# Kernel tuning notes

Hardware: AMD Instinct MI355X
Metric: run time of the kernel (lower is better)

The kernel has to match this reference:

```python
import jax, jax.numpy as jnp
import numpy as np

K = 8          # num groups
SIZE = 250     # state/hidden size (h1 = h2 = 250)
M = 576        # flattened input size (24x24)
B = 2048       # batch
HA = 100       # attention hidden
EPS = 1e-5


def _ln(x, g, b):
    mu = jnp.mean(x, axis=-1, keepdims=True)
    v = jnp.mean(jnp.square(x - mu), axis=-1, keepdims=True)
    return (x - mu) * jax.lax.rsqrt(v + EPS) * g + b


def setup_inputs() -> dict:
    key = jax.random.key(0)
    ks = jax.random.split(key, 10)
    def w(k, shape):
        return jax.random.normal(k, shape, jnp.float32) / np.sqrt(shape[0]).astype(np.float32)
    inp = {
        "x": jax.random.normal(ks[0], (B * K, M), jnp.float32),
        "state": jax.random.normal(ks[1], (B * K, SIZE), jnp.float32),
        # encoder: Linear(SIZE,250) + ReLU + LN(250)
        "enc_W": w(ks[2], (SIZE, 250)), "enc_b": jnp.zeros((250,), jnp.float32),
        "enc_g": jnp.ones((250,), jnp.float32), "enc_bt": jnp.zeros((250,), jnp.float32),
        # core: Linear(500,250) + ReLU + LN(250)
        "core_W": w(ks[3], (500, 250)), "core_b": jnp.zeros((250,), jnp.float32),
        "core_g": jnp.ones((250,), jnp.float32), "core_bt": jnp.zeros((250,), jnp.float32),
        # context: Linear(250,250) + ReLU + LN(250)
        "ctx_W": w(ks[4], (250, 250)), "ctx_b": jnp.zeros((250,), jnp.float32),
        "ctx_g": jnp.ones((250,), jnp.float32), "ctx_bt": jnp.zeros((250,), jnp.float32),
        # attention: Linear(250,100)+Tanh+LN(100)+Linear(100,1)+Sigmoid
        "att_W1": w(ks[5], (250, HA)), "att_b1": jnp.zeros((HA,), jnp.float32),
        "att_g": jnp.ones((HA,), jnp.float32), "att_bt": jnp.zeros((HA,), jnp.float32),
        "att_W2": w(ks[6], (HA, 1)), "att_b2": jnp.zeros((1,), jnp.float32),
        # output: Linear(250 + 250 + M, SIZE)
        "out_W": w(ks[7], (250 + 250 + M, SIZE)), "out_b": jnp.zeros((SIZE,), jnp.float32),
    }
    return inp


def reference(x, state, enc_W, enc_b, enc_g, enc_bt, core_W, core_b, core_g, core_bt,
              ctx_W, ctx_b, ctx_g, ctx_bt, att_W1, att_b1, att_g, att_bt,
              att_W2, att_b2, out_W, out_b):
    bk = state.shape[0]
    b = bk // K
    h1 = 250
    # 0-1. encode state -> [B*K, h1]
    s1 = _ln(jax.nn.relu(state @ enc_W + enc_b), enc_g, enc_bt)
    s1r = s1.reshape(b, K, h1)
    # 2-3. focus / context pairs via static gather index [K, K-1]
    idx = np.array([[j for j in range(K) if j != i] for i in range(K)], np.int32)
    cs = s1r[:, idx]                                    # [b, K, K-1, h1]
    fs = jnp.broadcast_to(s1r[:, :, None, :], cs.shape)  # [b, K, K-1, h1]
    # 4. concat pairs -> [b*K*(K-1), 2*h1]
    concat = jnp.concatenate([fs, cs], axis=-1).reshape(b * K * (K - 1), 2 * h1)
    # 5. core MLP
    core_out = _ln(jax.nn.relu(concat @ core_W + core_b), core_g, core_bt)
    # context MLP
    context_out = _ln(jax.nn.relu(core_out @ ctx_W + ctx_b), ctx_g, ctx_bt)
    # attention scalar per pair
    att_h = _ln(jnp.tanh(core_out @ att_W1 + att_b1), att_g, att_bt)
    att = jax.nn.sigmoid(att_h @ att_W2 + att_b2)        # [b*K*(K-1), 1]
    # 6-7. attention-weighted sum over K-1 context effects -> [B*K, h2]
    effect_sum = jnp.sum(context_out.reshape(bk, K - 1, h1) * att.reshape(bk, K - 1, 1), axis=1)
    # 8. decode
    total = jnp.concatenate([s1, effect_sum, x], axis=1)  # [B*K, h1+h2+M]
    new_state = total @ out_W + out_b                     # [B*K, SIZE]
    return new_state
```

## Files before the change

kernel.cpp:

```cpp
#include <hip/hip_runtime.h>
#include <math.h>

#define KK 8
#define H 250
#define MDIM 576
#define NB 2048
#define HA 100
#define ROWS (NB*KK)
#define PROWS (ROWS*7)
#define PQS 512
#define KP 1088
#define CSLD 352
#define EPS 1e-5f

typedef unsigned short ushort_t;
typedef short short8 __attribute__((ext_vector_type(8)));
typedef unsigned short us8 __attribute__((ext_vector_type(8)));
typedef unsigned short us4 __attribute__((ext_vector_type(4)));
typedef unsigned short us2 __attribute__((ext_vector_type(2)));
typedef float f32x4 __attribute__((ext_vector_type(4)));

__device__ __forceinline__ void wave_reduce2(float& a, float& b) {
#pragma unroll
    for (int m = 1; m < 64; m <<= 1) {
        a += __shfl_xor(a, m, 64);
        b += __shfl_xor(b, m, 64);
    }
}
__device__ __forceinline__ float wave_reduce1(float a) {
#pragma unroll
    for (int m = 1; m < 64; m <<= 1) a += __shfl_xor(a, m, 64);
    return a;
}

__device__ __forceinline__ void async_copy16(const void* g, void* l) {
    __builtin_amdgcn_global_load_lds(
        (const __attribute__((address_space(1))) void*)g,
        (__attribute__((address_space(3))) void*)l, 16, 0, 0);
}

__device__ __forceinline__ ushort_t f2bf(float v) {
    union { float f; unsigned int u; } c; c.f = v;
    unsigned int x = c.u;
    x += 0x7fff + ((x >> 16) & 1);
    return (ushort_t)(x >> 16);
}
__device__ __forceinline__ float bf2f(ushort_t v) {
    union { unsigned int u; float f; } c; c.u = ((unsigned int)v) << 16;
    return c.f;
}

__global__ __launch_bounds__(256) void k_prep(
    const float* __restrict__ out_W, const float* __restrict__ core_W,
    const float* __restrict__ ctx_W, const float* __restrict__ att_W1,
    const float* __restrict__ enc_W, const float* __restrict__ state,
    const float* __restrict__ x,
    ushort_t* __restrict__ Wt, ushort_t* __restrict__ Wpq,
    ushort_t* __restrict__ Wca, ushort_t* __restrict__ Wenc,
    ushort_t* __restrict__ Sb, ushort_t* __restrict__ Abuf)
{
    const int b = blockIdx.x, t = threadIdx.x;
    if (b < 256) {
        const int n = b;
        for (int k = t; k < KP; k += 256) {
            const float v = (n < H && k < 1076) ? out_W[(size_t)k * H + n] : 0.f;
            Wt[(size_t)n * KP + k] = f2bf(v);
        }
    } else if (b < 768) {
        const int n = b - 256, k = t;
        float v = 0.f;
        if (k < H) {
            if (n < H)                    v = core_W[(size_t)k * H + n];
            else if (n >= 256 && n < 506) v = core_W[(size_t)(H + k) * H + (n - 256)];
        }
        Wpq[(size_t)n * 256 + k] = f2bf(v);
    } else if (b < 1152) {
        const int n = b - 768, k = t;
        float v = 0.f;
        if (k < H) {
            if (n < H)           v = ctx_W[(size_t)k * H + n];
            else if (n < H + HA) v = att_W1[(size_t)k * HA + (n - H)];
        }
        Wca[(size_t)n * 256 + k] = f2bf(v);
    } else if (b < 1408) {
        const int n = b - 1152, k = t;
        const float v = (n < H && k < H) ? enc_W[(size_t)k * H + n] : 0.f;
        Wenc[(size_t)n * 256 + k] = f2bf(v);
    } else if (b < 2432) {
        const int r0 = (b - 1408) * 16;
        for (int idx = t; idx < 16 * 256; idx += 256) {
            const int r = r0 + (idx >> 8), k = idx & 255;
            const float v = (k < H) ? state[(size_t)r * H + k] : 0.f;
            Sb[(size_t)r * 256 + k] = f2bf(v);
        }
    } else {
        const int row = b - 2432;
        for (int c = 500 + t; c < KP; c += 256) {
            const float v = (c < 500 + MDIM) ? x[(size_t)row * MDIM + (c - 500)] : 0.f;
            Abuf[(size_t)row * KP + c] = f2bf(v);
        }
    }
}

__global__ __launch_bounds__(256) void k_gemm(
    const ushort_t* __restrict__ A, int lda,
    const ushort_t* __restrict__ B, int ldb,
    void* __restrict__ Cp, int ldc,
    const float* __restrict__ bias,
    int ksteps, int ntiles, int nlim, int bf16out)
{
    __shared__ __align__(16) ushort_t As[64 * 32];
    __shared__ __align__(16) ushort_t Bs[64 * 32];
    const int tid  = threadIdx.x;
    const int lane = tid & 63, wave = tid >> 6;
    const int wm = wave >> 1, wn = wave & 1;
    const int m0 = ((int)blockIdx.x / ntiles) * 64;
    const int n0 = ((int)blockIdx.x % ntiles) * 64;

    const int srow = tid >> 2;
    const int cs   = tid & 3;
    const int cl   = cs ^ ((srow >> 1) & 3);
    const ushort_t* gA = A + (size_t)(m0 + srow) * lda + cl * 8;
    const ushort_t* gB = B + (size_t)(n0 + srow) * ldb + cl * 8;
    ushort_t* lA = &As[tid * 8];
    ushort_t* lB = &Bs[tid * 8];

    const int q  = lane >> 4;
    const int fr = lane & 15;
    int aoff[2], boff[2];
#pragma unroll
    for (int s = 0; s < 2; ++s) {
        const int ra = wm * 32 + s * 16 + fr;
        aoff[s] = (ra * 4 + (q ^ ((ra >> 1) & 3))) * 8;
        const int rb = wn * 32 + s * 16 + fr;
        boff[s] = (rb * 4 + (q ^ ((rb >> 1) & 3))) * 8;
    }

    f32x4 acc[2][2] = {};
    for (int ks = 0; ks < ksteps; ++ks) {
        const int k0 = ks * 32;
        async_copy16(gA + k0, lA);
        async_copy16(gB + k0, lB);
        __syncthreads();
        short8 a[2], b[2];
#pragma unroll
        for (int s = 0; s < 2; ++s) {
            a[s] = *(const short8*)&As[aoff[s]];
            b[s] = *(const short8*)&Bs[boff[s]];
        }
#pragma unroll
        for (int ms = 0; ms < 2; ++ms)
#pragma unroll
            for (int ns = 0; ns < 2; ++ns)
                acc[ms][ns] = __builtin_amdgcn_mfma_f32_16x16x32_bf16(
                    a[ms], b[ns], acc[ms][ns], 0, 0, 0);
        __syncthreads();
    }

#pragma unroll
    for (int ms = 0; ms < 2; ++ms)
#pragma unroll
        for (int ns = 0; ns < 2; ++ns) {
            const int n_abs = n0 + wn * 32 + ns * 16 + fr;
            if (n_abs >= nlim) continue;
            const float bv = bias ? bias[n_abs] : 0.f;
#pragma unroll
            for (int reg = 0; reg < 4; ++reg) {
                const int m_abs = m0 + wm * 32 + ms * 16 + q * 4 + reg;
                const float v = acc[ms][ns][reg] + bv;
                if (bf16out) ((ushort_t*)Cp)[(size_t)m_abs * ldc + n_abs] = f2bf(v);
                else         ((float*)Cp)[(size_t)m_abs * ldc + n_abs] = v;
            }
        }
}

__global__ __launch_bounds__(256) void k_lnenc(const ushort_t* __restrict__ Epre,
    const float* __restrict__ eb, const float* __restrict__ eg,
    const float* __restrict__ ebt, ushort_t* __restrict__ Abuf)
{
    const int wave = threadIdx.x >> 6, lane = threadIdx.x & 63;
    const int row = blockIdx.x * 4 + wave;
    const int c0 = 4 * lane;

    const us4 v = *(const us4*)&Epre[(size_t)row * 256 + c0];
    float y[4]; float sm = 0.f, sq = 0.f;
#pragma unroll
    for (int t = 0; t < 4; ++t) {
        const int cc = c0 + t;
        float z = 0.f;
        if (cc < H) z = fmaxf(bf2f(v[t]) + eb[cc], 0.f);
        y[t] = z; sm += z; sq += z * z;
    }
    wave_reduce2(sm, sq);
    const float mu = sm * (1.f / H);
    const float rs = rsqrtf(sq * (1.f / H) - mu * mu + EPS);
    ushort_t o[4];
#pragma unroll
    for (int t = 0; t < 4; ++t) {
        const int cc = c0 + t;
        o[t] = (cc < H) ? f2bf((y[t] - mu) * rs * eg[cc] + ebt[cc]) : (ushort_t)0;
    }
    ushort_t* dst = Abuf + (size_t)row * KP + c0;
    if (c0 + 3 < H) { *(us4*)dst = (us4){o[0], o[1], o[2], o[3]}; }
    else {
        if (c0 + 1 < H) *(us2*)dst = (us2){o[0], o[1]};
    }
}

__global__ __launch_bounds__(256) void k_stats(const ushort_t* __restrict__ PQb,
    const float* __restrict__ core_b, float* __restrict__ Gstats)
{
    const int wave = threadIdx.x >> 6, lane = threadIdx.x & 63;
    const int g = blockIdx.x * 4 + wave;
    const int i = g & 7;
    const int c = lane * 4;

    const us4 pu = *(const us4*)&PQb[(size_t)g * PQS + c];
    float pe[4], cb[4]; bool vl[4];
#pragma unroll
    for (int t = 0; t < 4; ++t) {
        vl[t] = (c + t) < H;
        pe[t] = bf2f(pu[t]);
        cb[t] = vl[t] ? core_b[c + t] : 0.f;
    }
#pragma unroll 1
    for (int jj = 0; jj < 7; ++jj) {
        const int j = jj + (jj >= i ? 1 : 0);
        const int qr = (g & ~7) + j;
        const us4 qu = *(const us4*)&PQb[(size_t)qr * PQS + 256 + c];
        float sm = 0.f, sq = 0.f;
#pragma unroll
        for (int t = 0; t < 4; ++t) {
            const float z = vl[t] ? fmaxf(pe[t] + bf2f(qu[t]) + cb[t], 0.f) : 0.f;
            sm += z; sq += z * z;
        }
        wave_reduce2(sm, sq);
        if (lane == 0) {
            const int r = g * 7 + jj;
            const float mu = sm * (1.f / H);
            Gstats[r * 2]     = mu;
            Gstats[r * 2 + 1] = rsqrtf(sq * (1.f / H) - mu * mu + EPS);
        }
    }
}

__global__ __launch_bounds__(512, 4) void k_cs(
    const ushort_t* __restrict__ PQb, const float* __restrict__ Gstats,
    const float* __restrict__ core_b, const float* __restrict__ core_g,
    const float* __restrict__ core_bt,
    const ushort_t* __restrict__ Wca,
    ushort_t* __restrict__ Cs)
{
    __shared__ __align__(16) ushort_t As[64 * 32];
    __shared__ __align__(16) ushort_t Bs[384 * 32];
    const int tid = threadIdx.x, lane = tid & 63, wave = tid >> 6;
    const int wm = wave >> 2, wn = wave & 3;
    const int R0 = (int)blockIdx.x * 64;

    const int ar = tid >> 2, acb = tid & 3;
    const bool aon = tid < 256;
    int g = 0, qr = 0, apos = 0; float mu = 0.f, rs = 0.f;
    if (aon) {
        const int R = R0 + ar;
        g = R / 7; const int jj = R - g * 7;
        const int i = g & 7;
        const int j = jj + (jj >= i ? 1 : 0);
        qr = (g & ~7) + j;
        mu = Gstats[(size_t)R * 2]; rs = Gstats[(size_t)R * 2 + 1];
        apos = (ar * 4 + (acb ^ ((ar >> 1) & 3))) * 8;
    }
    const int q = lane >> 4, fr = lane & 15;

    f32x4 acc[2][6] = {};
    for (int ks = 0; ks < 8; ++ks) {
        const int k0 = ks * 32;
        if (aon) {
            const int kc = k0 + acb * 8;
            const us8 pu = *(const us8*)&PQb[(size_t)g  * PQS + kc];
            const us8 qu = *(const us8*)&PQb[(size_t)qr * PQS + 256 + kc];
            short8 ob;
#pragma unroll
            for (int e = 0; e < 8; ++e) {
                const int kk = kc + e;
                float v = 0.f;
                if (kk < H) {
                    const float z = fmaxf(bf2f(pu[e]) + bf2f(qu[e]) + core_b[kk], 0.f);
                    v = (z - mu) * rs * core_g[kk] + core_bt[kk];
                }
                ob[e] = (short)f2bf(v);
            }
            *(short8*)&As[apos] = ob;
        }
#pragma unroll
        for (int it = 0; it < 3; ++it) {
            const int ci  = it * 512 + tid;
            const int rb  = ci >> 2, cb2 = ci & 3;
            const int clb = cb2 ^ ((rb >> 1) & 3);
            async_copy16(Wca + (size_t)rb * 256 + k0 + clb * 8, &Bs[ci * 8]);
        }
        __syncthreads();
        short8 a[2];
#pragma unroll
        for (int ms = 0; ms < 2; ++ms) {
            const int row = wm * 32 + ms * 16 + fr;
            a[ms] = *(const short8*)&As[(row * 4 + (q ^ ((row >> 1) & 3))) * 8];
        }
#pragma unroll
        for (int nt = 0; nt < 6; ++nt) {
            const int n = wn * 96 + nt * 16 + fr;
            const short8 b = *(const short8*)&Bs[(n * 4 + (q ^ ((n >> 1) & 3))) * 8];
#pragma unroll
            for (int ms = 0; ms < 2; ++ms)
                acc[ms][nt] = __builtin_amdgcn_mfma_f32_16x16x32_bf16(
                    a[ms], b, acc[ms][nt], 0, 0, 0);
        }
        __syncthreads();
    }

#pragma unroll
    for (int ms = 0; ms < 2; ++ms)
#pragma unroll
        for (int nt = 0; nt < 6; ++nt) {
            const int col = wn * 96 + nt * 16 + fr;
            if (col >= CSLD) continue;
#pragma unroll
            for (int reg = 0; reg < 4; ++reg) {
                const int row = R0 + wm * 32 + ms * 16 + q * 4 + reg;
                Cs[(size_t)row * CSLD + col] = f2bf(acc[ms][nt][reg]);
            }
        }
}

__global__ __launch_bounds__(256) void k_eff(const ushort_t* __restrict__ Cs,
    const float* __restrict__ ctx_b, const float* __restrict__ ctx_g, const float* __restrict__ ctx_bt,
    const float* __restrict__ att_b1, const float* __restrict__ att_g, const float* __restrict__ att_bt,
    const float* __restrict__ attW2, const float* __restrict__ att_b2,
    ushort_t* __restrict__ Abuf)
{
    const int wave = threadIdx.x >> 6, lane = threadIdx.x & 63;
    const int g = blockIdx.x * 4 + wave;
    const int c0 = 4 * lane;
    const int c1 = 256 + 2 * lane;
    const bool l48 = lane < 48;

    int ce[6]; bool eC[6], eA[6]; float b_[6], g_[6], bt_[6], w2_[6];
#pragma unroll
    for (int e = 0; e < 6; ++e) {
        ce[e] = (e < 4) ? (c0 + e) : (c1 + (e - 4));
        const bool vld = (e < 4) || l48;
        eC[e] = vld && (ce[e] < H);
        eA[e] = vld && (ce[e] >= H) && (ce[e] < H + HA);
        if (eC[e])      { b_[e] = ctx_b[ce[e]]; g_[e] = ctx_g[ce[e]]; bt_[e] = ctx_bt[ce[e]]; w2_[e] = 0.f; }
        else if (eA[e]) { const int ca = ce[e] - H;
                          b_[e] = att_b1[ca]; g_[e] = att_g[ca]; bt_[e] = att_bt[ca]; w2_[e] = attW2[ca]; }
        else            { b_[e] = g_[e] = bt_[e] = w2_[e] = 0.f; }
    }
    const float ab2 = att_b2[0];
    float effa[4] = {0.f, 0.f, 0.f, 0.f};

#pragma unroll 1
    for (int jj = 0; jj < 7; ++jj) {
        const size_t base = ((size_t)g * 7 + jj) * CSLD;
        const us4 v0 = *(const us4*)&Cs[base + c0];
        us2 v1 = {0, 0};
        if (l48) v1 = *(const us2*)&Cs[base + c1];
        float raw[6];
#pragma unroll
        for (int e = 0; e < 4; ++e) raw[e] = bf2f(v0[e]);
        raw[4] = bf2f(v1[0]); raw[5] = bf2f(v1[1]);

        float sv[6]; float smc = 0.f, sqc = 0.f, sma = 0.f, sqa = 0.f;
#pragma unroll
        for (int e = 0; e < 6; ++e) {
            if (eC[e]) {
                const float z = fmaxf(raw[e] + b_[e], 0.f);
                sv[e] = z; smc += z; sqc += z * z;
            } else if (eA[e]) {
                const float za = tanhf(raw[e] + b_[e]);
                sv[e] = za; sma += za; sqa += za * za;
            } else sv[e] = 0.f;
        }
        wave_reduce2(smc, sqc);
        wave_reduce2(sma, sqa);
        const float muC = smc * (1.f / H);
        const float rsC = rsqrtf(sqc * (1.f / H) - muC * muC + EPS);
        const float muA = sma * (1.f / HA);
        const float rsA = rsqrtf(sqa * (1.f / HA) - muA * muA + EPS);
        float dot = 0.f;
#pragma unroll
        for (int e = 0; e < 6; ++e) {
            if (eA[e]) {
                const float ath = (sv[e] - muA) * rsA * g_[e] + bt_[e];
                dot += ath * w2_[e];
            }
        }
        dot = wave_reduce1(dot);
        const float ag = 1.f / (1.f + expf(-(dot + ab2)));
#pragma unroll
        for (int e = 0; e < 4; ++e) {
            if (eC[e]) {
                const float ctxo = (sv[e] - muC) * rsC * g_[e] + bt_[e];
                effa[e] = fmaf(ag, ctxo, effa[e]);
            }
        }
    }
    ushort_t* dst = Abuf + (size_t)g * KP + H + c0;
    if (c0 + 1 < H) *(us2*)dst       = (us2){f2bf(effa[0]), f2bf(effa[1])};
    if (c0 + 3 < H) *(us2*)(dst + 2) = (us2){f2bf(effa[2]), f2bf(effa[3])};
}

extern "C" void kernel_launch(void* const* d_in, const int* in_sizes, int n_in,
                              void* d_out, int out_size, void* d_ws, size_t ws_size,
                              hipStream_t stream)
{
    const float* x      = (const float*)d_in[0];
    const float* state  = (const float*)d_in[1];
    const float* enc_W  = (const float*)d_in[2];
    const float* enc_b  = (const float*)d_in[3];
    const float* enc_g  = (const float*)d_in[4];
    const float* enc_bt = (const float*)d_in[5];
    const float* core_W = (const float*)d_in[6];
    const float* core_b = (const float*)d_in[7];
    const float* core_g = (const float*)d_in[8];
    const float* core_bt= (const float*)d_in[9];
    const float* ctx_W  = (const float*)d_in[10];
    const float* ctx_b  = (const float*)d_in[11];
    const float* ctx_g  = (const float*)d_in[12];
    const float* ctx_bt = (const float*)d_in[13];
    const float* att_W1 = (const float*)d_in[14];
    const float* att_b1 = (const float*)d_in[15];
    const float* att_g  = (const float*)d_in[16];
    const float* att_bt = (const float*)d_in[17];
    const float* att_W2 = (const float*)d_in[18];
    const float* att_b2 = (const float*)d_in[19];
    const float* out_W  = (const float*)d_in[20];
    const float* out_b  = (const float*)d_in[21];
    float* out = (float*)d_out;

    ushort_t* Abuf = (ushort_t*)d_ws;
    ushort_t* Wt   = Abuf + (size_t)ROWS * KP;
    ushort_t* Wpq  = Wt + (size_t)256 * KP;
    ushort_t* Wca  = Wpq + (size_t)512 * 256;
    ushort_t* Wenc = Wca + (size_t)384 * 256;
    ushort_t* PQb  = Wenc + (size_t)256 * 256;
    float* Gstats  = (float*)(PQb + (size_t)ROWS * PQS);
    ushort_t* Cs   = (ushort_t*)(Gstats + (size_t)PROWS * 2);
    ushort_t* Sb   = Cs;
    ushort_t* Epre = Cs + (size_t)ROWS * 256;

    k_prep  <<<2432 + ROWS, 256, 0, stream>>>(out_W, core_W, ctx_W, att_W1, enc_W,
                                              state, x, Wt, Wpq, Wca, Wenc, Sb, Abuf);
    k_gemm  <<<(ROWS / 64) * 4, 256, 0, stream>>>(Sb, 256, Wenc, 256, Epre, 256,
                                                  nullptr, 8, 4, 256, 1);
    k_lnenc <<<ROWS / 4, 256, 0, stream>>>(Epre, enc_b, enc_g, enc_bt, Abuf);
    k_gemm  <<<(ROWS / 64) * 8, 256, 0, stream>>>(Abuf, KP, Wpq, 256, PQb, PQS,
                                                  nullptr, 8, 8, 512, 1);
    k_stats <<<ROWS / 4, 256, 0, stream>>>(PQb, core_b, Gstats);
    k_cs    <<<PROWS / 64, 512, 0, stream>>>(PQb, Gstats, core_b, core_g, core_bt,
                                             Wca, Cs);
    k_eff   <<<ROWS / 4, 256, 0, stream>>>(Cs, ctx_b, ctx_g, ctx_bt,
                                           att_b1, att_g, att_bt, att_W2, att_b2,
                                           Abuf);
    k_gemm  <<<(ROWS / 64) * 4, 256, 0, stream>>>(Abuf, KP, Wt, KP, out, H,
                                                  out_b, KP / 32, 4, H, 0);
}
```

Measured before the change: 375.6 us.

## Materialize normalized core activations in k_core instead of recomputing in GEMM

Before, the stats kernel wrote only per-pair mean and rstd, and the context/attention GEMM rebuilt the core LayerNorm output inside its A-tile load from P/Q rows. Now the stats kernel writes the full bf16 normalized core output for all 114688 pair rows, and the GEMM loads its A tiles with plain async copies. This takes the gather, ReLU, LN arithmetic and scalar weight loads out of the GEMM inner loop and lets A loads overlap like the B loads. In exchange it adds a write and re-read of a roughly 58 MB intermediate buffer and moves the workspace layout around.

```diff
diff --git a/kernel.cpp b/kernel.cpp
--- a/kernel.cpp
+++ b/kernel.cpp
@@ -207,8 +207,9 @@
     }
 }
 
-__global__ __launch_bounds__(256) void k_stats(const ushort_t* __restrict__ PQb,
-    const float* __restrict__ core_b, float* __restrict__ Gstats)
+__global__ __launch_bounds__(256) void k_core(const ushort_t* __restrict__ PQb,
+    const float* __restrict__ core_b, const float* __restrict__ core_g,
+    const float* __restrict__ core_bt, ushort_t* __restrict__ Co)
 {
     const int wave = threadIdx.x >> 6, lane = threadIdx.x & 63;
     const int g = blockIdx.x * 4 + wave;
@@ -216,38 +217,39 @@
     const int c = lane * 4;
 
     const us4 pu = *(const us4*)&PQb[(size_t)g * PQS + c];
-    float pe[4], cb[4]; bool vl[4];
+    float pe[4], cb[4], cg[4], cbt[4]; bool vl[4];
 #pragma unroll
     for (int t = 0; t < 4; ++t) {
-        vl[t] = (c + t) < H;
-        pe[t] = bf2f(pu[t]);
-        cb[t] = vl[t] ? core_b[c + t] : 0.f;
+        vl[t]  = (c + t) < H;
+        pe[t]  = bf2f(pu[t]);
+        cb[t]  = vl[t] ? core_b[c + t]  : 0.f;
+        cg[t]  = vl[t] ? core_g[c + t]  : 0.f;
+        cbt[t] = vl[t] ? core_bt[c + t] : 0.f;
     }
 #pragma unroll 1
     for (int jj = 0; jj < 7; ++jj) {
         const int j = jj + (jj >= i ? 1 : 0);
         const int qr = (g & ~7) + j;
         const us4 qu = *(const us4*)&PQb[(size_t)qr * PQS + 256 + c];
-        float sm = 0.f, sq = 0.f;
+        float z[4]; float sm = 0.f, sq = 0.f;
 #pragma unroll
         for (int t = 0; t < 4; ++t) {
-            const float z = vl[t] ? fmaxf(pe[t] + bf2f(qu[t]) + cb[t], 0.f) : 0.f;
-            sm += z; sq += z * z;
+            z[t] = vl[t] ? fmaxf(pe[t] + bf2f(qu[t]) + cb[t], 0.f) : 0.f;
+            sm += z[t]; sq += z[t] * z[t];
         }
         wave_reduce2(sm, sq);
-        if (lane == 0) {
-            const int r = g * 7 + jj;
-            const float mu = sm * (1.f / H);
-            Gstats[r * 2]     = mu;
-            Gstats[r * 2 + 1] = rsqrtf(sq * (1.f / H) - mu * mu + EPS);
-        }
+        const float mu = sm * (1.f / H);
+        const float rs = rsqrtf(sq * (1.f / H) - mu * mu + EPS);
+        us4 o;
+#pragma unroll
+        for (int t = 0; t < 4; ++t)
+            o[t] = vl[t] ? f2bf((z[t] - mu) * rs * cg[t] + cbt[t]) : (ushort_t)0;
+        *(us4*)&Co[((size_t)g * 7 + jj) * 256 + c] = o;
     }
 }
 
 __global__ __launch_bounds__(512, 4) void k_cs(
-    const ushort_t* __restrict__ PQb, const float* __restrict__ Gstats,
-    const float* __restrict__ core_b, const float* __restrict__ core_g,
-    const float* __restrict__ core_bt,
+    const ushort_t* __restrict__ Co,
     const ushort_t* __restrict__ Wca,
     ushort_t* __restrict__ Cs)
 {
@@ -259,38 +261,15 @@
 
     const int ar = tid >> 2, acb = tid & 3;
     const bool aon = tid < 256;
-    int g = 0, qr = 0, apos = 0; float mu = 0.f, rs = 0.f;
-    if (aon) {
-        const int R = R0 + ar;
-        g = R / 7; const int jj = R - g * 7;
-        const int i = g & 7;
-        const int j = jj + (jj >= i ? 1 : 0);
-        qr = (g & ~7) + j;
-        mu = Gstats[(size_t)R * 2]; rs = Gstats[(size_t)R * 2 + 1];
-        apos = (ar * 4 + (acb ^ ((ar >> 1) & 3))) * 8;
-    }
+    const int acl = acb ^ ((ar >> 1) & 3);
+    const ushort_t* gA = Co + (size_t)(R0 + ar) * 256 + acl * 8;
+
     const int q = lane >> 4, fr = lane & 15;
 
     f32x4 acc[2][6] = {};
     for (int ks = 0; ks < 8; ++ks) {
         const int k0 = ks * 32;
-        if (aon) {
-            const int kc = k0 + acb * 8;
-            const us8 pu = *(const us8*)&PQb[(size_t)g  * PQS + kc];
-            const us8 qu = *(const us8*)&PQb[(size_t)qr * PQS + 256 + kc];
-            short8 ob;
-#pragma unroll
-            for (int e = 0; e < 8; ++e) {
-                const int kk = kc + e;
-                float v = 0.f;
-                if (kk < H) {
-                    const float z = fmaxf(bf2f(pu[e]) + bf2f(qu[e]) + core_b[kk], 0.f);
-                    v = (z - mu) * rs * core_g[kk] + core_bt[kk];
-                }
-                ob[e] = (short)f2bf(v);
-            }
-            *(short8*)&As[apos] = ob;
-        }
+        if (aon) async_copy16(gA + k0, &As[tid * 8]);
 #pragma unroll
         for (int it = 0; it < 3; ++it) {
             const int ci  = it * 512 + tid;
@@ -442,11 +421,11 @@
     ushort_t* Wpq  = Wt + (size_t)256 * KP;
     ushort_t* Wca  = Wpq + (size_t)512 * 256;
     ushort_t* Wenc = Wca + (size_t)384 * 256;
-    ushort_t* PQb  = Wenc + (size_t)256 * 256;
-    float* Gstats  = (float*)(PQb + (size_t)ROWS * PQS);
-    ushort_t* Cs   = (ushort_t*)(Gstats + (size_t)PROWS * 2);
+    ushort_t* Co   = Wenc + (size_t)256 * 256;
+    ushort_t* Cs   = Co + (size_t)PROWS * 256;
     ushort_t* Sb   = Cs;
-    ushort_t* Epre = Cs + (size_t)ROWS * 256;
+    ushort_t* Epre = Sb + (size_t)ROWS * 256;
+    ushort_t* PQb  = Epre + (size_t)ROWS * 256;
 
     k_prep  <<<2432 + ROWS, 256, 0, stream>>>(out_W, core_W, ctx_W, att_W1, enc_W,
                                               state, x, Wt, Wpq, Wca, Wenc, Sb, Abuf);
@@ -455,9 +434,8 @@
     k_lnenc <<<ROWS / 4, 256, 0, stream>>>(Epre, enc_b, enc_g, enc_bt, Abuf);
     k_gemm  <<<(ROWS / 64) * 8, 256, 0, stream>>>(Abuf, KP, Wpq, 256, PQb, PQS,
                                                   nullptr, 8, 8, 512, 1);
-    k_stats <<<ROWS / 4, 256, 0, stream>>>(PQb, core_b, Gstats);
-    k_cs    <<<PROWS / 64, 512, 0, stream>>>(PQb, Gstats, core_b, core_g, core_bt,
-                                             Wca, Cs);
+    k_core  <<<ROWS / 4, 256, 0, stream>>>(PQb, core_b, core_g, core_bt, Co);
+    k_cs    <<<PROWS / 64, 512, 0, stream>>>(Co, Wca, Cs);
     k_eff   <<<ROWS / 4, 256, 0, stream>>>(Cs, ctx_b, ctx_g, ctx_bt,
                                            att_b1, att_g, att_bt, att_W2, att_b2,
                                            Abuf);
```

Result: faster. 351.6 us (-6.4%).
